# Optimization experiments

Hardware: AMD Instinct MI355X
Metric: run time of the kernel (lower is better)

The kernel has to match this reference:

```python
import jax, jax.numpy as jnp
import numpy as np

N_NODES = 100000
N_EDGES = 1600000
D_FEAT = 256


def _glorot(key, shape):
    fan_in = shape[0]
    return jax.random.normal(key, shape, jnp.float32) * (1.0 / np.sqrt(fan_in))


def setup_inputs() -> dict:
    key = jax.random.key(0)
    ks = jax.random.split(key, 8)
    return {
        "x": jax.random.normal(ks[0], (N_NODES, D_FEAT), jnp.float32),
        "edge_index": jax.random.randint(ks[1], (2, N_EDGES), 0, N_NODES, jnp.int32),
        "w1": _glorot(ks[2], (D_FEAT, 64)),
        "b1": jnp.zeros((64,), jnp.float32),
        "w2": _glorot(ks[3], (64, 32)),
        "b2": jnp.zeros((32,), jnp.float32),
        "wf1": _glorot(ks[4], (32, 16)),
        "bf1": jnp.zeros((16,), jnp.float32),
        "wf2": _glorot(ks[5], (16, 1)),
        "bf2": jnp.zeros((1,), jnp.float32),
    }


def reference(x, edge_index, w1, b1, w2, b2, wf1, bf1, wf2, bf2):
    n = x.shape[0]
    # GCNConv: add self-loops, symmetric D^{-1/2}(A+I)D^{-1/2} normalization
    loops = jnp.arange(n, dtype=edge_index.dtype)
    src = jnp.concatenate([edge_index[0], loops])  # message sources
    dst = jnp.concatenate([edge_index[1], loops])  # aggregation targets
    deg = jax.ops.segment_sum(jnp.ones_like(dst, x.dtype), dst, num_segments=n)
    dinv = jnp.where(deg > 0, jax.lax.rsqrt(jnp.maximum(deg, 1.0)), 0.0)
    norm = dinv[src] * dinv[dst]  # [E+N]

    def gcn_conv(h, W, b):
        hw = h @ W                                   # dense transform first (smaller msg dim)
        msg = hw[src] * norm[:, None]                # gather + scale
        return jax.ops.segment_sum(msg, dst, num_segments=n) + b  # scatter-add

    h = jax.nn.relu(gcn_conv(x, w1, b1))
    h = jax.nn.relu(gcn_conv(h, w2, b2))
    h = jax.nn.relu(h @ wf1 + bf1)
    out = h @ wf2 + bf2
    return out.squeeze(-1)  # [N]
```

## Files before the change

### kernel.cpp

```cpp
#include <hip/hip_runtime.h>
#include <cstdint>
#include <cstddef>

#define N_NODES 100000
#define N_EDGES 1600000

#define NBK   391
#define NPB   256
#define EPB   ((N_EDGES + NPB - 1) / NPB)
#define NSLOT (NBK * NPB)
#define NSB   ((NSLOT + 1023) / 1024)
#define ES_CAP (N_EDGES + NBK * 2048 + 64)

typedef __attribute__((ext_vector_type(8))) short bf16x8;
typedef __attribute__((ext_vector_type(4))) float f32x4;

__device__ __forceinline__ float b2f(unsigned short u) {
    return __uint_as_float(((unsigned)u) << 16);
}
__device__ __forceinline__ unsigned short f2b(float f) {
    unsigned x = __float_as_uint(f);
    return (unsigned short)((x + 0x7FFFu + ((x >> 16) & 1u)) >> 16);
}

__device__ __forceinline__ void split8(const float4& a0, const float4& a1,
                                       bf16x8& hi, bf16x8& lo) {
    float f[8] = {a0.x, a0.y, a0.z, a0.w, a1.x, a1.y, a1.z, a1.w};
#pragma unroll
    for (int j = 0; j < 8; ++j) {
        unsigned u = __float_as_uint(f[j]);
        hi[j] = (short)(u >> 16);
        float l = f[j] - __uint_as_float(u & 0xFFFF0000u);
        lo[j] = (short)(__float_as_uint(l) >> 16);
    }
}


__global__ __launch_bounds__(256) void k_hist(const int* __restrict__ dst,
                                              int* __restrict__ gcnt, int E) {
    __shared__ int lh[NBK];
    int t = threadIdx.x, bid = blockIdx.x;
    for (int i = t; i < NBK; i += 256) lh[i] = 0;
    __syncthreads();
    int e0 = bid * EPB, e1 = min(E, e0 + EPB);
    for (int e = e0 + t; e < e1; e += 256) atomicAdd(&lh[dst[e] >> 8], 1);
    __syncthreads();
    for (int b = t; b < NBK; b += 256) gcnt[b * NPB + bid] = lh[b];
}

__global__ __launch_bounds__(1024) void k_scanA(int* __restrict__ g,
                                                int* __restrict__ bsum, int ntot) {
    __shared__ int s[1024];
    int t = threadIdx.x;
    int i = blockIdx.x * 1024 + t;
    int v = (i < ntot) ? g[i] : 0;
    s[t] = v;
    __syncthreads();
    for (int o = 1; o < 1024; o <<= 1) {
        int a = (t >= o) ? s[t - o] : 0;
        __syncthreads();
        s[t] += a;
        __syncthreads();
    }
    if (i < ntot) g[i] = s[t] - v;
    if (t == 1023) bsum[blockIdx.x] = s[1023];
}

__global__ __launch_bounds__(128) void k_scanB(int* __restrict__ bsum, int nb) {
    __shared__ int s[128];
    int t = threadIdx.x;
    int v = (t < nb) ? bsum[t] : 0;
    s[t] = v;
    __syncthreads();
    for (int o = 1; o < 128; o <<= 1) {
        int a = (t >= o) ? s[t - o] : 0;
        __syncthreads();
        s[t] += a;
        __syncthreads();
    }
    if (t < nb) bsum[t] = s[t] - v;
}

__global__ __launch_bounds__(1024) void k_scanC(int* __restrict__ g,
                                                const int* __restrict__ bsum, int ntot) {
    int i = blockIdx.x * 1024 + threadIdx.x;
    if (i < ntot) g[i] += bsum[blockIdx.x];
}

__global__ __launch_bounds__(256) void k_partition(const int* __restrict__ src,
                                                   const int* __restrict__ dst,
                                                   const int* __restrict__ base,
                                                   unsigned* __restrict__ ebuf, int E) {
    __shared__ int lcur[NBK];
    int t = threadIdx.x, bid = blockIdx.x;
    for (int b = t; b < NBK; b += 256) lcur[b] = base[b * NPB + bid];
    __syncthreads();
    int e0 = bid * EPB, e1 = min(E, e0 + EPB);
    for (int e = e0 + t; e < e1; e += 256) {
        int d = dst[e];
        int b = d >> 8;
        int p = atomicAdd(&lcur[b], 1);
        ebuf[p] = (unsigned)src[e] | ((unsigned)(d & 255) << 20);
    }
}

__global__ __launch_bounds__(256) void k_bucket_csr(const int* __restrict__ base,
                                                    const unsigned* __restrict__ ebuf,
                                                    int* __restrict__ cnt,
                                                    float* __restrict__ dinv,
                                                    int* __restrict__ off,
                                                    int* __restrict__ es, int n) {
    __shared__ int lc[256];
    __shared__ int ss[256];
    __shared__ int lo[256];
    __shared__ int lcur[256];
    int b = blockIdx.x, t = threadIdx.x;
    int rstart = base[b * NPB];
    int rend = (b == NBK - 1) ? N_EDGES : base[(b + 1) * NPB];
    int wstart = ((rstart + 7) & ~7) + b * 2048;
    lc[t] = 0;
    __syncthreads();
    for (int e = rstart + t; e < rend; e += 256) atomicAdd(&lc[(int)(ebuf[e] >> 20)], 1);
    __syncthreads();
    int v = lc[t];
    int vp = (v + 7) & ~7;
    ss[t] = vp;
    __syncthreads();
    for (int o = 1; o < 256; o <<= 1) {
        int a = (t >= o) ? ss[t - o] : 0;
        __syncthreads();
        ss[t] += a;
        __syncthreads();
    }
    lo[t] = ss[t] - vp;
    lcur[t] = 0;
    int node = b * 256 + t;
    if (node < n) {
        cnt[node] = vp;
        dinv[node] = rsqrtf((float)v + 1.0f);
        off[node] = wstart + lo[t];
    }
    __syncthreads();
    for (int e = rstart + t; e < rend; e += 256) {
        unsigned u = ebuf[e];
        int l = (int)(u >> 20);
        int p = atomicAdd(&lcur[l], 1);
        es[wstart + lo[l] + p] = (int)(u & 0xFFFFFu);
    }
    for (int q = v; q < vp; ++q) es[wstart + lo[t] + q] = N_NODES;
}

__global__ void k_zero_sent(unsigned short* __restrict__ hwb1,
                            unsigned short* __restrict__ hwb2) {
    int t = threadIdx.x;
    if (t < 64) hwb1[(size_t)N_NODES * 64 + t] = 0;
    else hwb2[(size_t)N_NODES * 32 + (t - 64)] = 0;
}


__global__ __launch_bounds__(256) void k_gemm1_mfma(const float* __restrict__ x,
                                                    const float* __restrict__ w,
                                                    const float* __restrict__ dinv,
                                                    unsigned short* __restrict__ out, int M) {
    __shared__ unsigned short Bhi[32 * 64 * 8];
    __shared__ unsigned short Blo[32 * 64 * 8];
    int t = threadIdx.x;
    int wave = t >> 6, lane = t & 63;

    {
        int c = t & 63;
        int kg0 = t >> 6;
#pragma unroll
        for (int i = 0; i < 8; ++i) {
            int kgrp = kg0 + i * 4;
            bf16x8 h8, l8;
#pragma unroll
            for (int j = 0; j < 8; ++j) {
                float f = w[(size_t)(kgrp * 8 + j) * 64 + c];
                unsigned u = __float_as_uint(f);
                h8[j] = (short)(u >> 16);
                float l = f - __uint_as_float(u & 0xFFFF0000u);
                l8[j] = (short)(__float_as_uint(l) >> 16);
            }
            *(bf16x8*)&Bhi[(kgrp * 64 + c) * 8] = h8;
            *(bf16x8*)&Blo[(kgrp * 64 + c) * 8] = l8;
        }
    }
    __syncthreads();

    int row0w = blockIdx.x * 64 + wave * 16;
    int r = row0w + (lane & 15); if (r >= M) r = M - 1;
    const float* xr = x + (size_t)r * 256 + (lane >> 4) * 8;

    f32x4 acc[4] = {{0.f,0.f,0.f,0.f},{0.f,0.f,0.f,0.f},{0.f,0.f,0.f,0.f},{0.f,0.f,0.f,0.f}};

#pragma unroll
    for (int kf = 0; kf < 8; ++kf) {
        float4 a0 = *(const float4*)(xr + kf * 32);
        float4 a1 = *(const float4*)(xr + kf * 32 + 4);
        bf16x8 ahi, alo;
        split8(a0, a1, ahi, alo);
        int kgrpR = kf * 4 + (lane >> 4);
#pragma unroll
        for (int cf = 0; cf < 4; ++cf) {
            bf16x8 bhi = *(const bf16x8*)&Bhi[(kgrpR * 64 + cf * 16 + (lane & 15)) * 8];
            bf16x8 blo = *(const bf16x8*)&Blo[(kgrpR * 64 + cf * 16 + (lane & 15)) * 8];
            acc[cf] = __builtin_amdgcn_mfma_f32_16x16x32_bf16(ahi, bhi, acc[cf], 0, 0, 0);
            acc[cf] = __builtin_amdgcn_mfma_f32_16x16x32_bf16(ahi, blo, acc[cf], 0, 0, 0);
            acc[cf] = __builtin_amdgcn_mfma_f32_16x16x32_bf16(alo, bhi, acc[cf], 0, 0, 0);
        }
    }

#pragma unroll
    for (int j = 0; j < 4; ++j) {
        int rr = row0w + (lane >> 4) * 4 + j;
        if (rr < M) {
            float s = dinv[rr];
#pragma unroll
            for (int cf = 0; cf < 4; ++cf)
                out[(size_t)rr * 64 + cf * 16 + (lane & 15)] = f2b(acc[cf][j] * s);
        }
    }
}


__global__ __launch_bounds__(256) void k_gemm2_mfma(const float* __restrict__ h,
                                                    const float* __restrict__ w,
                                                    const float* __restrict__ dinv,
                                                    unsigned short* __restrict__ out, int M) {
    __shared__ unsigned short Bhi[8 * 32 * 8];
    __shared__ unsigned short Blo[8 * 32 * 8];
    int t = threadIdx.x;
    int wave = t >> 6, lane = t & 63;

    {
        int c = t & 31;
        int kg = t >> 5;
        bf16x8 h8, l8;
#pragma unroll
        for (int j = 0; j < 8; ++j) {
            float f = w[(size_t)(kg * 8 + j) * 32 + c];
            unsigned u = __float_as_uint(f);
            h8[j] = (short)(u >> 16);
            float l = f - __uint_as_float(u & 0xFFFF0000u);
            l8[j] = (short)(__float_as_uint(l) >> 16);
        }
        *(bf16x8*)&Bhi[(kg * 32 + c) * 8] = h8;
        *(bf16x8*)&Blo[(kg * 32 + c) * 8] = l8;
    }
    __syncthreads();

    int row0w = blockIdx.x * 64 + wave * 16;
    int r = row0w + (lane & 15); if (r >= M) r = M - 1;
    const float* xr = h + (size_t)r * 64 + (lane >> 4) * 8;

    f32x4 acc[2] = {{0.f,0.f,0.f,0.f},{0.f,0.f,0.f,0.f}};

#pragma unroll
    for (int kf = 0; kf < 2; ++kf) {
        float4 a0 = *(const float4*)(xr + kf * 32);
        float4 a1 = *(const float4*)(xr + kf * 32 + 4);
        bf16x8 ahi, alo;
        split8(a0, a1, ahi, alo);
        int kgrpR = kf * 4 + (lane >> 4);
#pragma unroll
        for (int cf = 0; cf < 2; ++cf) {
            bf16x8 bhi = *(const bf16x8*)&Bhi[(kgrpR * 32 + cf * 16 + (lane & 15)) * 8];
            bf16x8 blo = *(const bf16x8*)&Blo[(kgrpR * 32 + cf * 16 + (lane & 15)) * 8];
            acc[cf] = __builtin_amdgcn_mfma_f32_16x16x32_bf16(ahi, bhi, acc[cf], 0, 0, 0);
            acc[cf] = __builtin_amdgcn_mfma_f32_16x16x32_bf16(ahi, blo, acc[cf], 0, 0, 0);
            acc[cf] = __builtin_amdgcn_mfma_f32_16x16x32_bf16(alo, bhi, acc[cf], 0, 0, 0);
        }
    }

#pragma unroll
    for (int j = 0; j < 4; ++j) {
        int rr = row0w + (lane >> 4) * 4 + j;
        if (rr < M) {
            float s = dinv[rr];
#pragma unroll
            for (int cf = 0; cf < 2; ++cf)
                out[(size_t)rr * 32 + cf * 16 + (lane & 15)] = f2b(acc[cf][j] * s);
        }
    }
}


__global__ __launch_bounds__(256) void k_agg1(const unsigned short* __restrict__ hwb,
                                              const float* __restrict__ dinv,
                                              const int* __restrict__ cnt,
                                              const int* __restrict__ off,
                                              const int* __restrict__ es,
                                              const float* __restrict__ bias,
                                              float* __restrict__ hout) {
    int t = blockIdx.x * 256 + threadIdx.x;
    int node = t >> 6;
    int c = t & 63;
    float dn = dinv[node];
    float acc0 = b2f(hwb[(size_t)node * 64 + c]);
    float acc1 = 0.0f;
    const int* ep = es + off[node];
    int mp = cnt[node];
    for (int j = 0; j < mp; j += 8) {
        int4 e0 = *(const int4*)&ep[j];
        int4 e1 = *(const int4*)&ep[j + 4];
        float v0 = b2f(hwb[(size_t)e0.x * 64 + c]);
        float v1 = b2f(hwb[(size_t)e0.y * 64 + c]);
        float v2 = b2f(hwb[(size_t)e0.z * 64 + c]);
        float v3 = b2f(hwb[(size_t)e0.w * 64 + c]);
        float v4 = b2f(hwb[(size_t)e1.x * 64 + c]);
        float v5 = b2f(hwb[(size_t)e1.y * 64 + c]);
        float v6 = b2f(hwb[(size_t)e1.z * 64 + c]);
        float v7 = b2f(hwb[(size_t)e1.w * 64 + c]);
        acc0 += (v0 + v1) + (v2 + v3);
        acc1 += (v4 + v5) + (v6 + v7);
    }
    float acc = acc0 + acc1;
    hout[(size_t)node * 64 + c] = fmaxf(fmaf(dn, acc, bias[c]), 0.0f);
}


__global__ __launch_bounds__(256) void k_agg2_mlp(const unsigned short* __restrict__ hwb,
                                                  const float* __restrict__ dinv,
                                                  const int* __restrict__ cnt,
                                                  const int* __restrict__ off,
                                                  const int* __restrict__ es,
                                                  const float* __restrict__ bias2,
                                                  const float* __restrict__ wf1,
                                                  const float* __restrict__ bf1,
                                                  const float* __restrict__ wf2,
                                                  const float* __restrict__ bf2,
                                                  float* __restrict__ out) {
    __shared__ float hs[8][33];
    __shared__ float W1[512];
    __shared__ float B1[16];
    __shared__ float W2[16];
    int t = threadIdx.x;
    W1[t] = wf1[t];
    W1[t + 256] = wf1[t + 256];
    if (t < 16) { B1[t] = bf1[t]; W2[t] = wf2[t]; }

    int node0 = blockIdx.x * 8;
    int nl = t >> 5;
    int c = t & 31;
    int node = node0 + nl;
    float dn = dinv[node];
    float acc0 = b2f(hwb[(size_t)node * 32 + c]);
    float acc1 = 0.0f;
    const int* ep = es + off[node];
    int mp = cnt[node];
    for (int j = 0; j < mp; j += 8) {
        int4 e0 = *(const int4*)&ep[j];
        int4 e1 = *(const int4*)&ep[j + 4];
        float v0 = b2f(hwb[(size_t)e0.x * 32 + c]);
        float v1 = b2f(hwb[(size_t)e0.y * 32 + c]);
        float v2 = b2f(hwb[(size_t)e0.z * 32 + c]);
        float v3 = b2f(hwb[(size_t)e0.w * 32 + c]);
        float v4 = b2f(hwb[(size_t)e1.x * 32 + c]);
        float v5 = b2f(hwb[(size_t)e1.y * 32 + c]);
        float v6 = b2f(hwb[(size_t)e1.z * 32 + c]);
        float v7 = b2f(hwb[(size_t)e1.w * 32 + c]);
        acc0 += (v0 + v1) + (v2 + v3);
        acc1 += (v4 + v5) + (v6 + v7);
    }
    hs[nl][c] = fmaxf(fmaf(dn, acc0 + acc1, bias2[c]), 0.0f);
    __syncthreads();
    if (t < 128) {
        int nn = t >> 4, jj = t & 15;
        float s = B1[jj];
#pragma unroll
        for (int k = 0; k < 32; ++k) s += hs[nn][k] * W1[k * 16 + jj];
        float p = fmaxf(s, 0.0f) * W2[jj];
        p += __shfl_xor(p, 1);
        p += __shfl_xor(p, 2);
        p += __shfl_xor(p, 4);
        p += __shfl_xor(p, 8);
        if (jj == 0) out[node0 + nn] = p + bf2[0];
    }
}


extern "C" void kernel_launch(void* const* d_in, const int* in_sizes, int n_in,
                              void* d_out, int out_size, void* d_ws, size_t ws_size,
                              hipStream_t stream) {
    const float* x   = (const float*)d_in[0];
    const int*   ei  = (const int*)d_in[1];
    const float* w1  = (const float*)d_in[2];
    const float* b1  = (const float*)d_in[3];
    const float* w2  = (const float*)d_in[4];
    const float* b2  = (const float*)d_in[5];
    const float* wf1 = (const float*)d_in[6];
    const float* bf1 = (const float*)d_in[7];
    const float* wf2 = (const float*)d_in[8];
    const float* bf2 = (const float*)d_in[9];

    const int n = N_NODES;
    const int E = N_EDGES;
    const int* srcp = ei;
    const int* dstp = ei + E;

    char* p = (char*)d_ws;
    auto take = [&](size_t bytes) {
        char* r = p;
        p += (bytes + 255) & ~(size_t)255;
        return r;
    };
    float* dinv = (float*)take((size_t)n * 4);
    int*   cnt  = (int*)take((size_t)n * 4);
    int*   off  = (int*)take((size_t)n * 4);
    int*   gcnt = (int*)take((size_t)NSLOT * 4);
    int*   bsum = (int*)take(512);
    int*   es   = (int*)take((size_t)ES_CAP * 4);
    unsigned short* hwb1 = (unsigned short*)take((size_t)(n + 1) * 64 * 2);
    unsigned short* hwb2 = (unsigned short*)take((size_t)(n + 1) * 32 * 2);
    float* h1   = (float*)take((size_t)n * 64 * 4);
    unsigned* ebuf = (unsigned*)hwb1;

    k_zero_sent<<<1, 96, 0, stream>>>(hwb1, hwb2);
    k_hist<<<NPB, 256, 0, stream>>>(dstp, gcnt, E);
    k_scanA<<<NSB, 1024, 0, stream>>>(gcnt, bsum, NSLOT);
    k_scanB<<<1, 128, 0, stream>>>(bsum, NSB);
    k_scanC<<<NSB, 1024, 0, stream>>>(gcnt, bsum, NSLOT);
    k_partition<<<NPB, 256, 0, stream>>>(srcp, dstp, gcnt, ebuf, E);
    k_bucket_csr<<<NBK, 256, 0, stream>>>(gcnt, ebuf, cnt, dinv, off, es, n);

    k_gemm1_mfma<<<(n + 63) / 64, 256, 0, stream>>>(x, w1, dinv, hwb1, n);
    k_agg1<<<(n * 64) / 256, 256, 0, stream>>>(hwb1, dinv, cnt, off, es, b1, h1);
    k_gemm2_mfma<<<(n + 63) / 64, 256, 0, stream>>>(h1, w2, dinv, hwb2, n);
    k_agg2_mlp<<<n / 8, 256, 0, stream>>>(hwb2, dinv, cnt, off, es, b2,
                                          wf1, bf1, wf2, bf2, (float*)d_out);
}
```

Measured before the change: 178.8 us.

## Vectorize aggregation gathers, single-block scan, fold sentinel zeroing into histogram

In both aggregation kernels each lane now loads a group of four bf16 features with one 8-byte load, and different lane groups handle different edges; a cross-lane shuffle reduction then combines the partial sums. The aim is fewer, wider gather instructions per edge. The three-kernel scan is replaced by a single 1024-thread block that scans serial chunks, the partition count drops from 256 to 128, and the sentinel zeroing moves into k_hist, removing several launches. The costs are extra shuffle reduction work, idle lanes in the epilogue, more serial work in the single-block scan, and lower parallelism in the histogram and partition kernels.

```diff
diff --git a/kernel.cpp b/kernel.cpp
--- a/kernel.cpp
+++ b/kernel.cpp
@@ -6,10 +6,10 @@
 #define N_EDGES 1600000
 
 #define NBK   391
-#define NPB   256
+#define NPB   128
 #define EPB   ((N_EDGES + NPB - 1) / NPB)
 #define NSLOT (NBK * NPB)
-#define NSB   ((NSLOT + 1023) / 1024)
+#define SCH   ((NSLOT + 1023) / 1024)
 #define ES_CAP (N_EDGES + NBK * 2048 + 64)
 
 typedef __attribute__((ext_vector_type(8))) short bf16x8;
@@ -37,9 +37,15 @@
 
 
 __global__ __launch_bounds__(256) void k_hist(const int* __restrict__ dst,
-                                              int* __restrict__ gcnt, int E) {
+                                              int* __restrict__ gcnt,
+                                              unsigned short* __restrict__ hwb1,
+                                              unsigned short* __restrict__ hwb2, int E) {
     __shared__ int lh[NBK];
     int t = threadIdx.x, bid = blockIdx.x;
+    if (bid == 0) {
+        if (t < 64) hwb1[(size_t)N_NODES * 64 + t] = 0;
+        else if (t < 96) hwb2[(size_t)N_NODES * 32 + (t - 64)] = 0;
+    }
     for (int i = t; i < NBK; i += 256) lh[i] = 0;
     __syncthreads();
     int e0 = bid * EPB, e1 = min(E, e0 + EPB);
@@ -48,13 +54,16 @@
     for (int b = t; b < NBK; b += 256) gcnt[b * NPB + bid] = lh[b];
 }
 
-__global__ __launch_bounds__(1024) void k_scanA(int* __restrict__ g,
-                                                int* __restrict__ bsum, int ntot) {
+__global__ __launch_bounds__(1024) void k_scan1(int* __restrict__ g) {
     __shared__ int s[1024];
     int t = threadIdx.x;
-    int i = blockIdx.x * 1024 + t;
-    int v = (i < ntot) ? g[i] : 0;
-    s[t] = v;
+    int base = t * SCH;
+    int sum = 0;
+    for (int j = 0; j < SCH; ++j) {
+        int i = base + j;
+        if (i < NSLOT) sum += g[i];
+    }
+    s[t] = sum;
     __syncthreads();
     for (int o = 1; o < 1024; o <<= 1) {
         int a = (t >= o) ? s[t - o] : 0;
@@ -62,29 +71,11 @@
         s[t] += a;
         __syncthreads();
     }
-    if (i < ntot) g[i] = s[t] - v;
-    if (t == 1023) bsum[blockIdx.x] = s[1023];
-}
-
-__global__ __launch_bounds__(128) void k_scanB(int* __restrict__ bsum, int nb) {
-    __shared__ int s[128];
-    int t = threadIdx.x;
-    int v = (t < nb) ? bsum[t] : 0;
-    s[t] = v;
-    __syncthreads();
-    for (int o = 1; o < 128; o <<= 1) {
-        int a = (t >= o) ? s[t - o] : 0;
-        __syncthreads();
-        s[t] += a;
-        __syncthreads();
-    }
-    if (t < nb) bsum[t] = s[t] - v;
-}
-
-__global__ __launch_bounds__(1024) void k_scanC(int* __restrict__ g,
-                                                const int* __restrict__ bsum, int ntot) {
-    int i = blockIdx.x * 1024 + threadIdx.x;
-    if (i < ntot) g[i] += bsum[blockIdx.x];
+    int excl = s[t] - sum;
+    for (int j = 0; j < SCH; ++j) {
+        int i = base + j;
+        if (i < NSLOT) { int x = g[i]; g[i] = excl; excl += x; }
+    }
 }
 
 __global__ __launch_bounds__(256) void k_partition(const int* __restrict__ src,
@@ -150,13 +141,6 @@
     for (int q = v; q < vp; ++q) es[wstart + lo[t] + q] = N_NODES;
 }
 
-__global__ void k_zero_sent(unsigned short* __restrict__ hwb1,
-                            unsigned short* __restrict__ hwb2) {
-    int t = threadIdx.x;
-    if (t < 64) hwb1[(size_t)N_NODES * 64 + t] = 0;
-    else hwb2[(size_t)N_NODES * 32 + (t - 64)] = 0;
-}
-
 
 __global__ __launch_bounds__(256) void k_gemm1_mfma(const float* __restrict__ x,
                                                     const float* __restrict__ w,
@@ -293,30 +277,54 @@
                                               const int* __restrict__ es,
                                               const float* __restrict__ bias,
                                               float* __restrict__ hout) {
-    int t = blockIdx.x * 256 + threadIdx.x;
-    int node = t >> 6;
-    int c = t & 63;
-    float dn = dinv[node];
-    float acc0 = b2f(hwb[(size_t)node * 64 + c]);
-    float acc1 = 0.0f;
+    int gid = blockIdx.x * 256 + threadIdx.x;
+    int node = gid >> 6;
+    int lane = threadIdx.x & 63;
+    int q = lane >> 4;
+    int sub = lane & 15;
     const int* ep = es + off[node];
     int mp = cnt[node];
+    const unsigned short* hb = hwb + sub * 4;
+
+    float4 acc0 = {0.f, 0.f, 0.f, 0.f};
+    float4 acc1 = {0.f, 0.f, 0.f, 0.f};
     for (int j = 0; j < mp; j += 8) {
-        int4 e0 = *(const int4*)&ep[j];
-        int4 e1 = *(const int4*)&ep[j + 4];
-        float v0 = b2f(hwb[(size_t)e0.x * 64 + c]);
-        float v1 = b2f(hwb[(size_t)e0.y * 64 + c]);
-        float v2 = b2f(hwb[(size_t)e0.z * 64 + c]);
-        float v3 = b2f(hwb[(size_t)e0.w * 64 + c]);
-        float v4 = b2f(hwb[(size_t)e1.x * 64 + c]);
-        float v5 = b2f(hwb[(size_t)e1.y * 64 + c]);
-        float v6 = b2f(hwb[(size_t)e1.z * 64 + c]);
-        float v7 = b2f(hwb[(size_t)e1.w * 64 + c]);
-        acc0 += (v0 + v1) + (v2 + v3);
-        acc1 += (v4 + v5) + (v6 + v7);
-    }
-    float acc = acc0 + acc1;
-    hout[(size_t)node * 64 + c] = fmaxf(fmaf(dn, acc, bias[c]), 0.0f);
+        int sA = ep[j + q];
+        int sB = ep[j + 4 + q];
+        uint2 uA = *(const uint2*)(hb + (size_t)sA * 64);
+        uint2 uB = *(const uint2*)(hb + (size_t)sB * 64);
+        acc0.x += __uint_as_float(uA.x << 16);
+        acc0.y += __uint_as_float(uA.x & 0xFFFF0000u);
+        acc0.z += __uint_as_float(uA.y << 16);
+        acc0.w += __uint_as_float(uA.y & 0xFFFF0000u);
+        acc1.x += __uint_as_float(uB.x << 16);
+        acc1.y += __uint_as_float(uB.x & 0xFFFF0000u);
+        acc1.z += __uint_as_float(uB.y << 16);
+        acc1.w += __uint_as_float(uB.y & 0xFFFF0000u);
+    }
+    float ax = acc0.x + acc1.x;
+    float ay = acc0.y + acc1.y;
+    float az = acc0.z + acc1.z;
+    float aw = acc0.w + acc1.w;
+    ax += __shfl_xor(ax, 16); ax += __shfl_xor(ax, 32);
+    ay += __shfl_xor(ay, 16); ay += __shfl_xor(ay, 32);
+    az += __shfl_xor(az, 16); az += __shfl_xor(az, 32);
+    aw += __shfl_xor(aw, 16); aw += __shfl_xor(aw, 32);
+    if (q == 0) {
+        uint2 us = *(const uint2*)(hb + (size_t)node * 64);
+        ax += __uint_as_float(us.x << 16);
+        ay += __uint_as_float(us.x & 0xFFFF0000u);
+        az += __uint_as_float(us.y << 16);
+        aw += __uint_as_float(us.y & 0xFFFF0000u);
+        float dn = dinv[node];
+        float4 bb = *(const float4*)&bias[sub * 4];
+        float4 r;
+        r.x = fmaxf(fmaf(dn, ax, bb.x), 0.0f);
+        r.y = fmaxf(fmaf(dn, ay, bb.y), 0.0f);
+        r.z = fmaxf(fmaf(dn, az, bb.z), 0.0f);
+        r.w = fmaxf(fmaf(dn, aw, bb.w), 0.0f);
+        *(float4*)&hout[(size_t)node * 64 + sub * 4] = r;
+    }
 }
 
 
@@ -331,7 +339,7 @@
                                                   const float* __restrict__ wf2,
                                                   const float* __restrict__ bf2,
                                                   float* __restrict__ out) {
-    __shared__ float hs[8][33];
+    __shared__ float hs[4][36];
     __shared__ float W1[512];
     __shared__ float B1[16];
     __shared__ float W2[16];
@@ -340,32 +348,43 @@
     W1[t + 256] = wf1[t + 256];
     if (t < 16) { B1[t] = bf1[t]; W2[t] = wf2[t]; }
 
-    int node0 = blockIdx.x * 8;
-    int nl = t >> 5;
-    int c = t & 31;
-    int node = node0 + nl;
-    float dn = dinv[node];
-    float acc0 = b2f(hwb[(size_t)node * 32 + c]);
-    float acc1 = 0.0f;
+    int wv = t >> 6;
+    int lane = t & 63;
+    int o = lane >> 3;
+    int sub = lane & 7;
+    int node = blockIdx.x * 4 + wv;
     const int* ep = es + off[node];
     int mp = cnt[node];
+    const unsigned short* hb = hwb + sub * 4;
+
+    float4 acc = {0.f, 0.f, 0.f, 0.f};
     for (int j = 0; j < mp; j += 8) {
-        int4 e0 = *(const int4*)&ep[j];
-        int4 e1 = *(const int4*)&ep[j + 4];
-        float v0 = b2f(hwb[(size_t)e0.x * 32 + c]);
-        float v1 = b2f(hwb[(size_t)e0.y * 32 + c]);
-        float v2 = b2f(hwb[(size_t)e0.z * 32 + c]);
-        float v3 = b2f(hwb[(size_t)e0.w * 32 + c]);
-        float v4 = b2f(hwb[(size_t)e1.x * 32 + c]);
-        float v5 = b2f(hwb[(size_t)e1.y * 32 + c]);
-        float v6 = b2f(hwb[(size_t)e1.z * 32 + c]);
-        float v7 = b2f(hwb[(size_t)e1.w * 32 + c]);
-        acc0 += (v0 + v1) + (v2 + v3);
-        acc1 += (v4 + v5) + (v6 + v7);
-    }
-    hs[nl][c] = fmaxf(fmaf(dn, acc0 + acc1, bias2[c]), 0.0f);
-    __syncthreads();
-    if (t < 128) {
+        int s = ep[j + o];
+        uint2 u = *(const uint2*)(hb + (size_t)s * 32);
+        acc.x += __uint_as_float(u.x << 16);
+        acc.y += __uint_as_float(u.x & 0xFFFF0000u);
+        acc.z += __uint_as_float(u.y << 16);
+        acc.w += __uint_as_float(u.y & 0xFFFF0000u);
+    }
+    acc.x += __shfl_xor(acc.x, 8); acc.x += __shfl_xor(acc.x, 16); acc.x += __shfl_xor(acc.x, 32);
+    acc.y += __shfl_xor(acc.y, 8); acc.y += __shfl_xor(acc.y, 16); acc.y += __shfl_xor(acc.y, 32);
+    acc.z += __shfl_xor(acc.z, 8); acc.z += __shfl_xor(acc.z, 16); acc.z += __shfl_xor(acc.z, 32);
+    acc.w += __shfl_xor(acc.w, 8); acc.w += __shfl_xor(acc.w, 16); acc.w += __shfl_xor(acc.w, 32);
+    if (o == 0) {
+        uint2 us = *(const uint2*)(hb + (size_t)node * 32);
+        acc.x += __uint_as_float(us.x << 16);
+        acc.y += __uint_as_float(us.x & 0xFFFF0000u);
+        acc.z += __uint_as_float(us.y << 16);
+        acc.w += __uint_as_float(us.y & 0xFFFF0000u);
+        float dn = dinv[node];
+        float4 bb = *(const float4*)&bias2[sub * 4];
+        hs[wv][sub * 4 + 0] = fmaxf(fmaf(dn, acc.x, bb.x), 0.0f);
+        hs[wv][sub * 4 + 1] = fmaxf(fmaf(dn, acc.y, bb.y), 0.0f);
+        hs[wv][sub * 4 + 2] = fmaxf(fmaf(dn, acc.z, bb.z), 0.0f);
+        hs[wv][sub * 4 + 3] = fmaxf(fmaf(dn, acc.w, bb.w), 0.0f);
+    }
+    __syncthreads();
+    if (t < 64) {
         int nn = t >> 4, jj = t & 15;
         float s = B1[jj];
 #pragma unroll
@@ -375,7 +394,7 @@
         p += __shfl_xor(p, 2);
         p += __shfl_xor(p, 4);
         p += __shfl_xor(p, 8);
-        if (jj == 0) out[node0 + nn] = p + bf2[0];
+        if (jj == 0) out[blockIdx.x * 4 + nn] = p + bf2[0];
     }
 }
 
@@ -409,24 +428,20 @@
     int*   cnt  = (int*)take((size_t)n * 4);
     int*   off  = (int*)take((size_t)n * 4);
     int*   gcnt = (int*)take((size_t)NSLOT * 4);
-    int*   bsum = (int*)take(512);
     int*   es   = (int*)take((size_t)ES_CAP * 4);
     unsigned short* hwb1 = (unsigned short*)take((size_t)(n + 1) * 64 * 2);
     unsigned short* hwb2 = (unsigned short*)take((size_t)(n + 1) * 32 * 2);
     float* h1   = (float*)take((size_t)n * 64 * 4);
     unsigned* ebuf = (unsigned*)hwb1;
 
-    k_zero_sent<<<1, 96, 0, stream>>>(hwb1, hwb2);
-    k_hist<<<NPB, 256, 0, stream>>>(dstp, gcnt, E);
-    k_scanA<<<NSB, 1024, 0, stream>>>(gcnt, bsum, NSLOT);
-    k_scanB<<<1, 128, 0, stream>>>(bsum, NSB);
-    k_scanC<<<NSB, 1024, 0, stream>>>(gcnt, bsum, NSLOT);
+    k_hist<<<NPB, 256, 0, stream>>>(dstp, gcnt, hwb1, hwb2, E);
+    k_scan1<<<1, 1024, 0, stream>>>(gcnt);
     k_partition<<<NPB, 256, 0, stream>>>(srcp, dstp, gcnt, ebuf, E);
     k_bucket_csr<<<NBK, 256, 0, stream>>>(gcnt, ebuf, cnt, dinv, off, es, n);
 
     k_gemm1_mfma<<<(n + 63) / 64, 256, 0, stream>>>(x, w1, dinv, hwb1, n);
     k_agg1<<<(n * 64) / 256, 256, 0, stream>>>(hwb1, dinv, cnt, off, es, b1, h1);
     k_gemm2_mfma<<<(n + 63) / 64, 256, 0, stream>>>(h1, w2, dinv, hwb2, n);
-    k_agg2_mlp<<<n / 8, 256, 0, stream>>>(hwb2, dinv, cnt, off, es, b2,
+    k_agg2_mlp<<<n / 4, 256, 0, stream>>>(hwb2, dinv, cnt, off, es, b2,
                                           wf1, bf1, wf2, bf2, (float*)d_out);
 }
```

New measurement: 292.5 us. +63.6%, slower.
